# Performance work log

Measured on AMD Instinct MI355X. Metric: run time of the kernel, lower is better.

## Reference

```python
import jax, jax.numpy as jnp
import numpy as np

N_EMBD = 384
NUM_HEADS = 6
HEAD_SIZE = 64


def setup_inputs() -> dict:
    key = jax.random.key(0)
    ks = jax.random.split(key, 6)
    B, T = 128, 256
    D = NUM_HEADS * HEAD_SIZE  # 384
    x = jax.random.normal(ks[0], (B, T, N_EMBD), dtype=jnp.float32)
    Wk = jax.random.normal(ks[1], (N_EMBD, D), dtype=jnp.float32) * (N_EMBD ** -0.5)
    Wq = jax.random.normal(ks[2], (N_EMBD, D), dtype=jnp.float32) * (N_EMBD ** -0.5)
    Wv = jax.random.normal(ks[3], (N_EMBD, D), dtype=jnp.float32) * (N_EMBD ** -0.5)
    Wp = jax.random.normal(ks[4], (D, N_EMBD), dtype=jnp.float32) * (D ** -0.5)
    bp = jax.random.normal(ks[5], (N_EMBD,), dtype=jnp.float32) * 0.01
    return {"x": x, "Wk": Wk, "Wq": Wq, "Wv": Wv, "Wp": Wp, "bp": bp}


def reference(x, Wk, Wq, Wv, Wp, bp):
    B, T, C = x.shape
    H, hs = NUM_HEADS, HEAD_SIZE
    # QKV projections -> [B, H, T, hs]
    q = (x @ Wq).reshape(B, T, H, hs).transpose(0, 2, 1, 3)
    k = (x @ Wk).reshape(B, T, H, hs).transpose(0, 2, 1, 3)
    v = (x @ Wv).reshape(B, T, H, hs).transpose(0, 2, 1, 3)
    # NOTE: original scales by C**-0.5 where C = n_embd (not head_size)
    scale = jnp.asarray(C, x.dtype) ** -0.5
    wei = jnp.einsum('bhtd,bhsd->bhts', q, k) * scale  # [B, H, T, T]
    causal = jnp.tril(jnp.ones((T, T), dtype=bool))
    wei = jnp.where(causal, wei, -jnp.inf)
    wei = jax.nn.softmax(wei, axis=-1)
    # dropout disabled (eval mode) for deterministic reference
    out = jnp.einsum('bhts,bhsd->bhtd', wei, v)  # [B, H, T, hs]
    out = out.transpose(0, 2, 1, 3).reshape(B, T, H * hs)
    return out @ Wp + bp
```

## Files before the change

kernel.cpp:

```cpp
#include <hip/hip_runtime.h>
#include <hip/hip_bf16.h>


#define T_SEQ 256
#define NH 6
#define HS 64
#define CIN 384
#define BATCH 128
#define BT (BATCH * T_SEQ)
#define ELEMS ((size_t)BT * CIN)

using f32x4  = __attribute__((ext_vector_type(4))) float;
using bf16x8 = __attribute__((ext_vector_type(8))) short;

typedef __attribute__((address_space(3))) void       lds_vp;
typedef __attribute__((address_space(1))) const void glob_vp;

static __device__ __forceinline__ unsigned short f2bf(float f) {
  union { float f; unsigned u; } v; v.f = f;
  unsigned r = v.u + 0x7FFFu + ((v.u >> 16) & 1u);
  return (unsigned short)(r >> 16);
}

static __device__ __forceinline__ bf16x8 ld_bf8(const unsigned short* p) {
  return *reinterpret_cast<const bf16x8*>(p);
}

static __device__ __forceinline__ void gl_lds16(const void* g, void* l) {
  __builtin_amdgcn_global_load_lds((glob_vp*)g, (lds_vp*)l, 16, 0, 0);
}

__global__ __launch_bounds__(256) void convert_x(
    const float* __restrict__ x, unsigned short* __restrict__ xb)
{
  size_t i = (((size_t)blockIdx.x << 8) + threadIdx.x) << 3;
  float4 f0 = *reinterpret_cast<const float4*>(x + i);
  float4 f1 = *reinterpret_cast<const float4*>(x + i + 4);
  uint4 pk;
  pk.x = f2bf(f0.x) | ((unsigned)f2bf(f0.y) << 16);
  pk.y = f2bf(f0.z) | ((unsigned)f2bf(f0.w) << 16);
  pk.z = f2bf(f1.x) | ((unsigned)f2bf(f1.y) << 16);
  pk.w = f2bf(f1.z) | ((unsigned)f2bf(f1.w) << 16);
  *reinterpret_cast<uint4*>(xb + i) = pk;
}

__global__ __launch_bounds__(256) void convert_wqkv(
    const float* __restrict__ Wq, const float* __restrict__ Wk,
    const float* __restrict__ Wv, unsigned short* __restrict__ dst)
{
  __shared__ float t[32][33];
  const int z = blockIdx.z;
  const float* __restrict__ W = (z == 0) ? Wq : (z == 1) ? Wk : Wv;
  const int tx = threadIdx.x & 31, ty = threadIdx.x >> 5;
  const int k0 = blockIdx.x * 32, n0 = blockIdx.y * 32;
#pragma unroll
  for (int i = 0; i < 4; ++i)
    t[ty + 8 * i][tx] = W[(size_t)(k0 + ty + 8 * i) * CIN + n0 + tx];
  __syncthreads();
#pragma unroll
  for (int i = 0; i < 4; ++i)
    dst[((size_t)z * CIN + n0 + ty + 8 * i) * CIN + k0 + tx] =
        f2bf(t[tx][ty + 8 * i]);
}

__global__ __launch_bounds__(256) void transpose_w(
    const float* __restrict__ W, unsigned short* __restrict__ dst)
{
  __shared__ float t[32][33];
  const int tx = threadIdx.x & 31, ty = threadIdx.x >> 5;
  const int k0 = blockIdx.x * 32, n0 = blockIdx.y * 32;
#pragma unroll
  for (int i = 0; i < 4; ++i)
    t[ty + 8 * i][tx] = W[(size_t)(k0 + ty + 8 * i) * CIN + n0 + tx];
  __syncthreads();
#pragma unroll
  for (int i = 0; i < 4; ++i)
    dst[((size_t)(n0 + ty + 8 * i)) * CIN + k0 + tx] = f2bf(t[tx][ty + 8 * i]);
}

__global__ __launch_bounds__(256) void gemm_qkv(
    const unsigned short* __restrict__ xb,
    const unsigned short* __restrict__ wt,
    unsigned short* __restrict__ q_ws, unsigned short* __restrict__ k_ws,
    unsigned short* __restrict__ vT_ws)
{
  __shared__ __align__(16) unsigned short XA[2][128][64];
  __shared__ __align__(16) unsigned short XB[2][128][64];

  const int tid = threadIdx.x;
  const int w = tid >> 6, l = tid & 63, g = l >> 4, c = l & 15;
  const int wr = w >> 1, wc = w & 1;

  const int wid = ((int)blockIdx.x & 7) * 288 + ((int)blockIdx.x >> 3);
  const int n_t = wid % 9, m_t = wid / 9;
  const int m0 = m_t * 128, n0 = n_t * 128;

  f32x4 acc[4][4];
#pragma unroll
  for (int mi = 0; mi < 4; ++mi)
#pragma unroll
    for (int nj = 0; nj < 4; ++nj) { f32x4 zz = {0.f,0.f,0.f,0.f}; acc[mi][nj] = zz; }

  const int lrow = l >> 3;
  const int lchk = (l & 7) ^ lrow;
  const char* ga = (const char*)xb +
      ((size_t)(m0 + w * 32 + lrow) * CIN + lchk * 8) * 2;
  const char* gb = (const char*)wt +
      ((size_t)(n0 + w * 32 + lrow) * CIN + lchk * 8) * 2;

#define STAGE_QKV(buf, k0)                                              \
  {                                                                     \
    _Pragma("unroll")                                                   \
    for (int i_ = 0; i_ < 4; ++i_) {                                    \
      gl_lds16(ga + ((k0) + i_ * 8 * CIN) * 2, &XA[buf][w * 32 + i_ * 8][0]); \
      gl_lds16(gb + ((k0) + i_ * 8 * CIN) * 2, &XB[buf][w * 32 + i_ * 8][0]); \
    }                                                                   \
  }

  STAGE_QKV(0, 0);
  __syncthreads();

  int cur = 0;
  for (int t = 0; t < 6; ++t) {
    if (t < 5) STAGE_QKV(cur ^ 1, (t + 1) * 64);
#pragma unroll
    for (int kk = 0; kk < 2; ++kk) {
      bf16x8 a[4], b[4];
#pragma unroll
      for (int mi = 0; mi < 4; ++mi) {
        const int row = wr * 64 + mi * 16 + c;
        a[mi] = *reinterpret_cast<const bf16x8*>(
            (const char*)&XA[cur][row][0] + (((kk * 4 + g) ^ (c & 7)) << 4));
      }
#pragma unroll
      for (int nj = 0; nj < 4; ++nj) {
        const int row = wc * 64 + nj * 16 + c;
        b[nj] = *reinterpret_cast<const bf16x8*>(
            (const char*)&XB[cur][row][0] + (((kk * 4 + g) ^ (c & 7)) << 4));
      }
#pragma unroll
      for (int mi = 0; mi < 4; ++mi)
#pragma unroll
        for (int nj = 0; nj < 4; ++nj)
          acc[mi][nj] = __builtin_amdgcn_mfma_f32_16x16x32_bf16(
              a[mi], b[nj], acc[mi][nj], 0, 0, 0);
    }
    __syncthreads();
    cur ^= 1;
  }

  const int z = n_t / 3;
  const int colw = (n_t % 3) * 128 + wc * 64;
  const int h = colw >> 6;
  const int b = m0 >> 8;
  const int trow0 = (m0 & 255) + wr * 64;

  if (z == 2) {
#pragma unroll
    for (int nj = 0; nj < 4; ++nj) {
      const int d = nj * 16 + c;
#pragma unroll
      for (int mi = 0; mi < 4; ++mi) {
        const int t0 = trow0 + mi * 16 + 4 * g;
        ushort4 pk;
        pk.x = f2bf(acc[mi][nj][0]); pk.y = f2bf(acc[mi][nj][1]);
        pk.z = f2bf(acc[mi][nj][2]); pk.w = f2bf(acc[mi][nj][3]);
        *reinterpret_cast<ushort4*>(
            vT_ws + (((size_t)b * NH + h) * HS + d) * T_SEQ + t0) = pk;
      }
    }
  } else {
    unsigned short* dstb = (z == 0) ? q_ws : k_ws;
    char* OS = (char*)XA + w * 8192;
#pragma unroll
    for (int nj = 0; nj < 4; ++nj)
#pragma unroll
      for (int mi = 0; mi < 4; ++mi)
#pragma unroll
        for (int i = 0; i < 4; ++i) {
          const int r = mi * 16 + 4 * g + i;
          const int chk = (nj * 2 + (c >> 3)) ^ (r & 7);
          *reinterpret_cast<unsigned short*>(
              OS + r * 128 + (chk << 4) + (c & 7) * 2) = f2bf(acc[mi][nj][i]);
        }
    __syncthreads();
    unsigned short* gdst = dstb + (((size_t)b * NH + h) * T_SEQ + trow0) * HS;
#pragma unroll
    for (int p = 0; p < 8; ++p) {
      const int r = p * 8 + (l >> 3);
      const int chk = (l & 7) ^ (r & 7);
      uint4 v = *reinterpret_cast<const uint4*>(OS + r * 128 + (chk << 4));
      *reinterpret_cast<uint4*>((char*)gdst + r * 128 + (l & 7) * 16) = v;
    }
  }
#undef STAGE_QKV
}

template<int NT>
__device__ __forceinline__ void attn_tile(
    const unsigned short* __restrict__ qg,
    const unsigned short* KL, const unsigned short* VL,
    unsigned short* __restrict__ o_ws, int bh, int qt, int g, int c)
{
  const int q0 = qt * 16;
  const int kxor = (c & 7) << 4;

  const char* qrow = (const char*)qg + (size_t)(q0 + c) * 128;
  const bf16x8 qb0 = *reinterpret_cast<const bf16x8*>(qrow + g * 16);
  const bf16x8 qb1 = *reinterpret_cast<const bf16x8*>(qrow + 64 + g * 16);

  f32x4 s[NT];
#pragma unroll
  for (int kt = 0; kt < NT; ++kt) {
    const char* krow = (const char*)KL + (kt * 16 + c) * 128;
    bf16x8 ka0 = *reinterpret_cast<const bf16x8*>(krow + ((g * 16) ^ kxor));
    bf16x8 ka1 = *reinterpret_cast<const bf16x8*>(krow + ((64 + g * 16) ^ kxor));
    f32x4 z = {0.f, 0.f, 0.f, 0.f};
    z = __builtin_amdgcn_mfma_f32_16x16x32_bf16(ka0, qb0, z, 0, 0, 0);
    z = __builtin_amdgcn_mfma_f32_16x16x32_bf16(ka1, qb1, z, 0, 0, 0);
    s[kt] = z;
  }

  const float sc = 0.07362372251839260f;
  float mx = -1e30f;
#pragma unroll
  for (int kt = 0; kt < NT; ++kt)
#pragma unroll
    for (int i = 0; i < 4; ++i) {
      const int k = kt * 16 + 4 * g + i;
      float v = (k <= q0 + c) ? s[kt][i] * sc : -1e30f;
      s[kt][i] = v;
      mx = fmaxf(mx, v);
    }
  mx = fmaxf(mx, __shfl_xor(mx, 16));
  mx = fmaxf(mx, __shfl_xor(mx, 32));

  float sum = 0.f;
#pragma unroll
  for (int kt = 0; kt < NT; ++kt)
#pragma unroll
    for (int i = 0; i < 4; ++i) {
      float p = __builtin_exp2f(s[kt][i] - mx);
      s[kt][i] = p;
      sum += p;
    }
  sum += __shfl_xor(sum, 16);
  sum += __shfl_xor(sum, 32);
  const float inv = 1.0f / sum;

  unsigned pk0[NT], pk1[NT];
#pragma unroll
  for (int kt = 0; kt < NT; ++kt) {
    float2 p01 = {s[kt][0] * inv, s[kt][1] * inv};
    float2 p23 = {s[kt][2] * inv, s[kt][3] * inv};
    __hip_bfloat162 b01 = __float22bfloat162_rn(p01);
    __hip_bfloat162 b23 = __float22bfloat162_rn(p23);
    pk0[kt] = *reinterpret_cast<unsigned*>(&b01);
    pk1[kt] = *reinterpret_cast<unsigned*>(&b23);
  }

  f32x4 acc[4];
#pragma unroll
  for (int nt = 0; nt < 4; ++nt) { f32x4 zz = {0.f,0.f,0.f,0.f}; acc[nt] = zz; }

  const int srcA = ((g & 1) << 5) + c;
  const int srcB = srcA + 16;
  const bool hi = (g >= 2);
#pragma unroll
  for (int ks = 0; ks < NT / 2; ++ks) {
    unsigned a0A = __shfl(pk0[2 * ks],     srcA);
    unsigned a1A = __shfl(pk1[2 * ks],     srcA);
    unsigned a0B = __shfl(pk0[2 * ks],     srcB);
    unsigned a1B = __shfl(pk1[2 * ks],     srcB);
    unsigned b0A = __shfl(pk0[2 * ks + 1], srcA);
    unsigned b1A = __shfl(pk1[2 * ks + 1], srcA);
    unsigned b0B = __shfl(pk0[2 * ks + 1], srcB);
    unsigned b1B = __shfl(pk1[2 * ks + 1], srcB);
    union { unsigned u[4]; bf16x8 v; } pa;
    pa.u[0] = hi ? b0A : a0A;
    pa.u[1] = hi ? b1A : a1A;
    pa.u[2] = hi ? b0B : a0B;
    pa.u[3] = hi ? b1B : a1B;
#pragma unroll
    for (int nt = 0; nt < 4; ++nt) {
      const char* vrow = (const char*)VL + (nt * 16 + c) * 512;
      bf16x8 vb = *reinterpret_cast<const bf16x8*>(
          vrow + ((ks * 64 + g * 16) ^ kxor));
      acc[nt] = __builtin_amdgcn_mfma_f32_16x16x32_bf16(pa.v, vb, acc[nt], 0, 0, 0);
    }
  }

  const int b = bh / NH, h = bh % NH;
  unsigned short* ob = o_ws + ((size_t)(b * T_SEQ + q0)) * CIN + h * HS;
#pragma unroll
  for (int nt = 0; nt < 4; ++nt)
#pragma unroll
    for (int i = 0; i < 4; ++i)
      ob[(size_t)(4 * g + i) * CIN + nt * 16 + c] = f2bf(acc[nt][i]);
}

__global__ __launch_bounds__(512, 4) void attn_kernel(
    const unsigned short* __restrict__ q_ws,
    const unsigned short* __restrict__ k_ws,
    const unsigned short* __restrict__ vT_ws,
    unsigned short* __restrict__ o_ws)
{
  __shared__ __align__(16) unsigned short KL[256 * 64];
  __shared__ __align__(16) unsigned short VL[64 * 256];

  const int tid = threadIdx.x;
  const int w = tid >> 6, l = tid & 63, g = l >> 4, c = l & 15;
  const int bh = blockIdx.x;

  const char* kg = (const char*)(k_ws + (size_t)bh * T_SEQ * HS);
  const char* vg = (const char*)(vT_ws + (size_t)bh * HS * T_SEQ);
#pragma unroll
  for (int i = 0; i < 4; ++i) {
    const int cid = i * 512 + w * 64 + l;
    const int rk = cid >> 3, pk_ = cid & 7;
    gl_lds16(kg + rk * 128 + ((pk_ ^ (rk & 7)) << 4),
             (char*)KL + (size_t)(i * 512 + w * 64) * 16);
    const int rv = cid >> 5, pv = cid & 31;
    const int sv = (pv & ~7) | ((pv & 7) ^ (rv & 7));
    gl_lds16(vg + rv * 512 + (sv << 4),
             (char*)VL + (size_t)(i * 512 + w * 64) * 16);
  }
  __syncthreads();

  const unsigned short* qg = q_ws + (size_t)bh * T_SEQ * HS;
  switch (w) {
    case 0: attn_tile<2>(qg, KL, VL, o_ws, bh, 0, g, c);
            attn_tile<16>(qg, KL, VL, o_ws, bh, 15, g, c); break;
    case 1: attn_tile<2>(qg, KL, VL, o_ws, bh, 1, g, c);
            attn_tile<16>(qg, KL, VL, o_ws, bh, 14, g, c); break;
    case 2: attn_tile<4>(qg, KL, VL, o_ws, bh, 2, g, c);
            attn_tile<14>(qg, KL, VL, o_ws, bh, 13, g, c); break;
    case 3: attn_tile<4>(qg, KL, VL, o_ws, bh, 3, g, c);
            attn_tile<14>(qg, KL, VL, o_ws, bh, 12, g, c); break;
    case 4: attn_tile<6>(qg, KL, VL, o_ws, bh, 4, g, c);
            attn_tile<12>(qg, KL, VL, o_ws, bh, 11, g, c); break;
    case 5: attn_tile<6>(qg, KL, VL, o_ws, bh, 5, g, c);
            attn_tile<12>(qg, KL, VL, o_ws, bh, 10, g, c); break;
    case 6: attn_tile<8>(qg, KL, VL, o_ws, bh, 6, g, c);
            attn_tile<10>(qg, KL, VL, o_ws, bh, 9, g, c); break;
    case 7: attn_tile<8>(qg, KL, VL, o_ws, bh, 7, g, c);
            attn_tile<10>(qg, KL, VL, o_ws, bh, 8, g, c); break;
  }
}

__global__ __launch_bounds__(256) void proj_kernel(
    const unsigned short* __restrict__ ob,
    const unsigned short* __restrict__ wpt,
    const float* __restrict__ bp,
    float* __restrict__ out)
{
  __shared__ __align__(16) unsigned short XA[2][128][64];
  __shared__ __align__(16) unsigned short XB[2][128][64];

  const int tid = threadIdx.x;
  const int w = tid >> 6, l = tid & 63, g = l >> 4, c = l & 15;
  const int wr = w >> 1, wc = w & 1;

  const int wid = ((int)blockIdx.x & 7) * 96 + ((int)blockIdx.x >> 3);
  const int n_t = wid % 3, m_t = wid / 3;
  const int m0 = m_t * 128, n0 = n_t * 128;

  f32x4 acc[4][4];
#pragma unroll
  for (int mi = 0; mi < 4; ++mi)
#pragma unroll
    for (int nj = 0; nj < 4; ++nj) { f32x4 zz = {0.f,0.f,0.f,0.f}; acc[mi][nj] = zz; }

  const int lrow = l >> 3;
  const int lchk = (l & 7) ^ lrow;
  const char* ga = (const char*)ob +
      ((size_t)(m0 + w * 32 + lrow) * CIN + lchk * 8) * 2;
  const char* gb = (const char*)wpt +
      ((size_t)(n0 + w * 32 + lrow) * CIN + lchk * 8) * 2;

#define STAGE_PRJ(buf, k0)                                              \
  {                                                                     \
    _Pragma("unroll")                                                   \
    for (int i_ = 0; i_ < 4; ++i_) {                                    \
      gl_lds16(ga + ((k0) + i_ * 8 * CIN) * 2, &XA[buf][w * 32 + i_ * 8][0]); \
      gl_lds16(gb + ((k0) + i_ * 8 * CIN) * 2, &XB[buf][w * 32 + i_ * 8][0]); \
    }                                                                   \
  }

  STAGE_PRJ(0, 0);
  __syncthreads();

  int cur = 0;
  for (int t = 0; t < 6; ++t) {
    if (t < 5) STAGE_PRJ(cur ^ 1, (t + 1) * 64);
#pragma unroll
    for (int kk = 0; kk < 2; ++kk) {
      bf16x8 a[4], b[4];
#pragma unroll
      for (int mi = 0; mi < 4; ++mi) {
        const int row = wr * 64 + mi * 16 + c;
        a[mi] = *reinterpret_cast<const bf16x8*>(
            (const char*)&XA[cur][row][0] + (((kk * 4 + g) ^ (c & 7)) << 4));
      }
#pragma unroll
      for (int nj = 0; nj < 4; ++nj) {
        const int row = wc * 64 + nj * 16 + c;
        b[nj] = *reinterpret_cast<const bf16x8*>(
            (const char*)&XB[cur][row][0] + (((kk * 4 + g) ^ (c & 7)) << 4));
      }
#pragma unroll
      for (int mi = 0; mi < 4; ++mi)
#pragma unroll
        for (int nj = 0; nj < 4; ++nj)
          acc[mi][nj] = __builtin_amdgcn_mfma_f32_16x16x32_bf16(
              a[mi], b[nj], acc[mi][nj], 0, 0, 0);
    }
    __syncthreads();
    cur ^= 1;
  }

#pragma unroll
  for (int nj = 0; nj < 4; ++nj) {
    const int col = n0 + wc * 64 + nj * 16 + c;
    const float bias = bp[col];
#pragma unroll
    for (int mi = 0; mi < 4; ++mi) {
      const int mrow = m0 + wr * 64 + mi * 16 + 4 * g;
#pragma unroll
      for (int i = 0; i < 4; ++i)
        out[(size_t)(mrow + i) * CIN + col] = acc[mi][nj][i] + bias;
    }
  }
#undef STAGE_PRJ
}

extern "C" void kernel_launch(void* const* d_in, const int* in_sizes, int n_in,
                              void* d_out, int out_size, void* d_ws, size_t ws_size,
                              hipStream_t stream)
{
  const float* x  = (const float*)d_in[0];
  const float* Wk = (const float*)d_in[1];
  const float* Wq = (const float*)d_in[2];
  const float* Wv = (const float*)d_in[3];
  const float* Wp = (const float*)d_in[4];
  const float* bp = (const float*)d_in[5];
  float* out = (float*)d_out;

  unsigned short* ws    = (unsigned short*)d_ws;
  unsigned short* xb_o  = ws;
  unsigned short* q_ws  = ws + ELEMS;
  unsigned short* k_ws  = ws + 2 * ELEMS;
  unsigned short* vT_ws = ws + 3 * ELEMS;
  unsigned short* wqkvT = (unsigned short*)d_out;

  convert_x   <<<6144, 256, 0, stream>>>(x, xb_o);
  convert_wqkv<<<dim3(12, 12, 3), 256, 0, stream>>>(Wq, Wk, Wv, wqkvT);
  gemm_qkv    <<<2304, 256, 0, stream>>>(xb_o, wqkvT, q_ws, k_ws, vT_ws);
  attn_kernel <<<BATCH * NH, 512, 0, stream>>>(q_ws, k_ws, vT_ws, xb_o);
  transpose_w <<<dim3(12, 12), 256, 0, stream>>>(Wp, q_ws);
  proj_kernel <<<768, 256, 0, stream>>>(xb_o, q_ws, bp, out);
}
```

Measured before the change: 119.9 us.

## Single-buffer GEMM LDS tiles and raise wave priority around MFMA blocks

Both GEMM kernels drop double-buffered LDS staging in favour of a single 32KB buffer: each k-step loads, syncs, computes and syncs again. This halves LDS use per block so more blocks can be resident per CU, relying on inter-block overlap to hide load latency instead of intra-block prefetch. s_setprio(1) is also wrapped around the MFMA sequences in the GEMMs and the attention tile to favour issuing matrix ops. The risk is exposed global-to-LDS latency within each block when occupancy does not rise enough to cover it.

```diff
diff --git a/kernel.cpp b/kernel.cpp
--- a/kernel.cpp
+++ b/kernel.cpp
@@ -84,8 +84,7 @@
     unsigned short* __restrict__ q_ws, unsigned short* __restrict__ k_ws,
     unsigned short* __restrict__ vT_ws)
 {
-  __shared__ __align__(16) unsigned short XA[2][128][64];
-  __shared__ __align__(16) unsigned short XB[2][128][64];
+  __shared__ __align__(16) unsigned short SM[2][128][64];
 
   const int tid = threadIdx.x;
   const int w = tid >> 6, l = tid & 63, g = l >> 4, c = l & 15;
@@ -108,21 +107,13 @@
   const char* gb = (const char*)wt +
       ((size_t)(n0 + w * 32 + lrow) * CIN + lchk * 8) * 2;
 
-#define STAGE_QKV(buf, k0)                                              \
-  {                                                                     \
-    _Pragma("unroll")                                                   \
-    for (int i_ = 0; i_ < 4; ++i_) {                                    \
-      gl_lds16(ga + ((k0) + i_ * 8 * CIN) * 2, &XA[buf][w * 32 + i_ * 8][0]); \
-      gl_lds16(gb + ((k0) + i_ * 8 * CIN) * 2, &XB[buf][w * 32 + i_ * 8][0]); \
-    }                                                                   \
-  }
-
-  STAGE_QKV(0, 0);
-  __syncthreads();
-
-  int cur = 0;
   for (int t = 0; t < 6; ++t) {
-    if (t < 5) STAGE_QKV(cur ^ 1, (t + 1) * 64);
+#pragma unroll
+    for (int i_ = 0; i_ < 4; ++i_) {
+      gl_lds16(ga + (t * 64 + i_ * 8 * CIN) * 2, &SM[0][w * 32 + i_ * 8][0]);
+      gl_lds16(gb + (t * 64 + i_ * 8 * CIN) * 2, &SM[1][w * 32 + i_ * 8][0]);
+    }
+    __syncthreads();
 #pragma unroll
     for (int kk = 0; kk < 2; ++kk) {
       bf16x8 a[4], b[4];
@@ -130,23 +121,24 @@
       for (int mi = 0; mi < 4; ++mi) {
         const int row = wr * 64 + mi * 16 + c;
         a[mi] = *reinterpret_cast<const bf16x8*>(
-            (const char*)&XA[cur][row][0] + (((kk * 4 + g) ^ (c & 7)) << 4));
+            (const char*)&SM[0][row][0] + (((kk * 4 + g) ^ (c & 7)) << 4));
       }
 #pragma unroll
       for (int nj = 0; nj < 4; ++nj) {
         const int row = wc * 64 + nj * 16 + c;
         b[nj] = *reinterpret_cast<const bf16x8*>(
-            (const char*)&XB[cur][row][0] + (((kk * 4 + g) ^ (c & 7)) << 4));
+            (const char*)&SM[1][row][0] + (((kk * 4 + g) ^ (c & 7)) << 4));
       }
+      __builtin_amdgcn_s_setprio(1);
 #pragma unroll
       for (int mi = 0; mi < 4; ++mi)
 #pragma unroll
         for (int nj = 0; nj < 4; ++nj)
           acc[mi][nj] = __builtin_amdgcn_mfma_f32_16x16x32_bf16(
               a[mi], b[nj], acc[mi][nj], 0, 0, 0);
+      __builtin_amdgcn_s_setprio(0);
     }
     __syncthreads();
-    cur ^= 1;
   }
 
   const int z = n_t / 3;
@@ -171,7 +163,7 @@
     }
   } else {
     unsigned short* dstb = (z == 0) ? q_ws : k_ws;
-    char* OS = (char*)XA + w * 8192;
+    char* OS = (char*)SM + w * 8192;
 #pragma unroll
     for (int nj = 0; nj < 4; ++nj)
 #pragma unroll
@@ -193,7 +185,6 @@
       *reinterpret_cast<uint4*>((char*)gdst + r * 128 + (l & 7) * 16) = v;
     }
   }
-#undef STAGE_QKV
 }
 
 template<int NT>
@@ -216,8 +207,10 @@
     bf16x8 ka0 = *reinterpret_cast<const bf16x8*>(krow + ((g * 16) ^ kxor));
     bf16x8 ka1 = *reinterpret_cast<const bf16x8*>(krow + ((64 + g * 16) ^ kxor));
     f32x4 z = {0.f, 0.f, 0.f, 0.f};
+    __builtin_amdgcn_s_setprio(1);
     z = __builtin_amdgcn_mfma_f32_16x16x32_bf16(ka0, qb0, z, 0, 0, 0);
     z = __builtin_amdgcn_mfma_f32_16x16x32_bf16(ka1, qb1, z, 0, 0, 0);
+    __builtin_amdgcn_s_setprio(0);
     s[kt] = z;
   }
 
@@ -281,6 +274,7 @@
     pa.u[1] = hi ? b1A : a1A;
     pa.u[2] = hi ? b0B : a0B;
     pa.u[3] = hi ? b1B : a1B;
+    __builtin_amdgcn_s_setprio(1);
 #pragma unroll
     for (int nt = 0; nt < 4; ++nt) {
       const char* vrow = (const char*)VL + (nt * 16 + c) * 512;
@@ -288,6 +282,7 @@
           vrow + ((ks * 64 + g * 16) ^ kxor));
       acc[nt] = __builtin_amdgcn_mfma_f32_16x16x32_bf16(pa.v, vb, acc[nt], 0, 0, 0);
     }
+    __builtin_amdgcn_s_setprio(0);
   }
 
   const int b = bh / NH, h = bh % NH;
@@ -354,8 +349,7 @@
     const float* __restrict__ bp,
     float* __restrict__ out)
 {
-  __shared__ __align__(16) unsigned short XA[2][128][64];
-  __shared__ __align__(16) unsigned short XB[2][128][64];
+  __shared__ __align__(16) unsigned short SM[2][128][64];
 
   const int tid = threadIdx.x;
   const int w = tid >> 6, l = tid & 63, g = l >> 4, c = l & 15;
@@ -378,21 +372,13 @@
   const char* gb = (const char*)wpt +
       ((size_t)(n0 + w * 32 + lrow) * CIN + lchk * 8) * 2;
 
-#define STAGE_PRJ(buf, k0)                                              \
-  {                                                                     \
-    _Pragma("unroll")                                                   \
-    for (int i_ = 0; i_ < 4; ++i_) {                                    \
-      gl_lds16(ga + ((k0) + i_ * 8 * CIN) * 2, &XA[buf][w * 32 + i_ * 8][0]); \
-      gl_lds16(gb + ((k0) + i_ * 8 * CIN) * 2, &XB[buf][w * 32 + i_ * 8][0]); \
-    }                                                                   \
-  }
-
-  STAGE_PRJ(0, 0);
-  __syncthreads();
-
-  int cur = 0;
   for (int t = 0; t < 6; ++t) {
-    if (t < 5) STAGE_PRJ(cur ^ 1, (t + 1) * 64);
+#pragma unroll
+    for (int i_ = 0; i_ < 4; ++i_) {
+      gl_lds16(ga + (t * 64 + i_ * 8 * CIN) * 2, &SM[0][w * 32 + i_ * 8][0]);
+      gl_lds16(gb + (t * 64 + i_ * 8 * CIN) * 2, &SM[1][w * 32 + i_ * 8][0]);
+    }
+    __syncthreads();
 #pragma unroll
     for (int kk = 0; kk < 2; ++kk) {
       bf16x8 a[4], b[4];
@@ -400,23 +386,24 @@
       for (int mi = 0; mi < 4; ++mi) {
         const int row = wr * 64 + mi * 16 + c;
         a[mi] = *reinterpret_cast<const bf16x8*>(
-            (const char*)&XA[cur][row][0] + (((kk * 4 + g) ^ (c & 7)) << 4));
+            (const char*)&SM[0][row][0] + (((kk * 4 + g) ^ (c & 7)) << 4));
       }
 #pragma unroll
       for (int nj = 0; nj < 4; ++nj) {
         const int row = wc * 64 + nj * 16 + c;
         b[nj] = *reinterpret_cast<const bf16x8*>(
-            (const char*)&XB[cur][row][0] + (((kk * 4 + g) ^ (c & 7)) << 4));
+            (const char*)&SM[1][row][0] + (((kk * 4 + g) ^ (c & 7)) << 4));
       }
+      __builtin_amdgcn_s_setprio(1);
 #pragma unroll
       for (int mi = 0; mi < 4; ++mi)
 #pragma unroll
         for (int nj = 0; nj < 4; ++nj)
           acc[mi][nj] = __builtin_amdgcn_mfma_f32_16x16x32_bf16(
               a[mi], b[nj], acc[mi][nj], 0, 0, 0);
+      __builtin_amdgcn_s_setprio(0);
     }
     __syncthreads();
-    cur ^= 1;
   }
 
 #pragma unroll
@@ -431,7 +418,6 @@
         out[(size_t)(mrow + i) * CIN + col] = acc[mi][nj][i] + bias;
     }
   }
-#undef STAGE_PRJ
 }
 
 extern "C" void kernel_launch(void* const* d_in, const int* in_sizes, int n_in,
```

New measurement: 115.8 us. 3.4% less time.

## Fuse fp32-to-bf16 conversion of x into QKV GEMM A-tile loads; add MFMA priority hints

Applied to the files above, without the earlier changes.

Drops the standalone convert_x kernel. The QKV GEMM now loads fp32 x into registers, packs it to bf16 and writes it into swizzled LDS after the MFMAs, while B still uses direct global-to-LDS loads. This removes one kernel launch and a full bf16 write and read of x. In exchange, each of the nine N-tiles rereads fp32 x (twice the bytes) and register pressure rises. It also wraps the MFMA sections in s_setprio in the GEMMs and the attention kernel.

```diff
diff --git a/kernel.cpp b/kernel.cpp
--- a/kernel.cpp
+++ b/kernel.cpp
@@ -22,26 +22,17 @@
   return (unsigned short)(r >> 16);
 }
 
-static __device__ __forceinline__ bf16x8 ld_bf8(const unsigned short* p) {
-  return *reinterpret_cast<const bf16x8*>(p);
-}
-
-static __device__ __forceinline__ void gl_lds16(const void* g, void* l) {
-  __builtin_amdgcn_global_load_lds((glob_vp*)g, (lds_vp*)l, 16, 0, 0);
-}
-
-__global__ __launch_bounds__(256) void convert_x(
-    const float* __restrict__ x, unsigned short* __restrict__ xb)
-{
-  size_t i = (((size_t)blockIdx.x << 8) + threadIdx.x) << 3;
-  float4 f0 = *reinterpret_cast<const float4*>(x + i);
-  float4 f1 = *reinterpret_cast<const float4*>(x + i + 4);
+static __device__ __forceinline__ uint4 pack8(float4 f0, float4 f1) {
   uint4 pk;
   pk.x = f2bf(f0.x) | ((unsigned)f2bf(f0.y) << 16);
   pk.y = f2bf(f0.z) | ((unsigned)f2bf(f0.w) << 16);
   pk.z = f2bf(f1.x) | ((unsigned)f2bf(f1.y) << 16);
   pk.w = f2bf(f1.z) | ((unsigned)f2bf(f1.w) << 16);
-  *reinterpret_cast<uint4*>(xb + i) = pk;
+  return pk;
+}
+
+static __device__ __forceinline__ void gl_lds16(const void* g, void* l) {
+  __builtin_amdgcn_global_load_lds((glob_vp*)g, (lds_vp*)l, 16, 0, 0);
 }
 
 __global__ __launch_bounds__(256) void convert_wqkv(
@@ -79,13 +70,13 @@
 }
 
 __global__ __launch_bounds__(256) void gemm_qkv(
-    const unsigned short* __restrict__ xb,
+    const float* __restrict__ x,
     const unsigned short* __restrict__ wt,
     unsigned short* __restrict__ q_ws, unsigned short* __restrict__ k_ws,
     unsigned short* __restrict__ vT_ws)
 {
-  __shared__ __align__(16) unsigned short XA[2][128][64];
-  __shared__ __align__(16) unsigned short XB[2][128][64];
+  __shared__ __align__(16) unsigned short A [2][128][64];
+  __shared__ __align__(16) unsigned short Bt[2][128][64];
 
   const int tid = threadIdx.x;
   const int w = tid >> 6, l = tid & 63, g = l >> 4, c = l & 15;
@@ -101,28 +92,45 @@
 #pragma unroll
     for (int nj = 0; nj < 4; ++nj) { f32x4 zz = {0.f,0.f,0.f,0.f}; acc[mi][nj] = zz; }
 
-  const int lrow = l >> 3;
-  const int lchk = (l & 7) ^ lrow;
-  const char* ga = (const char*)xb +
-      ((size_t)(m0 + w * 32 + lrow) * CIN + lchk * 8) * 2;
+  const int lr = l >> 3;
+  const int cc = l & 7;
+  const float* gax = x + (size_t)(m0 + w * 32 + lr) * CIN + cc * 8;
   const char* gb = (const char*)wt +
-      ((size_t)(n0 + w * 32 + lrow) * CIN + lchk * 8) * 2;
-
-#define STAGE_QKV(buf, k0)                                              \
-  {                                                                     \
-    _Pragma("unroll")                                                   \
-    for (int i_ = 0; i_ < 4; ++i_) {                                    \
-      gl_lds16(ga + ((k0) + i_ * 8 * CIN) * 2, &XA[buf][w * 32 + i_ * 8][0]); \
-      gl_lds16(gb + ((k0) + i_ * 8 * CIN) * 2, &XB[buf][w * 32 + i_ * 8][0]); \
-    }                                                                   \
-  }
-
-  STAGE_QKV(0, 0);
+      ((size_t)(n0 + w * 32 + lr) * CIN + ((cc ^ lr) << 3)) * 2;
+
+#define ISSUE_B(buf, t)                                                  \
+  _Pragma("unroll")                                                      \
+  for (int i_ = 0; i_ < 4; ++i_)                                         \
+    gl_lds16(gb + ((t) * 64 + i_ * 8 * CIN) * 2, &Bt[buf][w * 32 + i_ * 8][0]);
+
+#define LOAD_A(reg, t)                                                   \
+  _Pragma("unroll")                                                      \
+  for (int i_ = 0; i_ < 4; ++i_) {                                       \
+    reg[i_][0] = *reinterpret_cast<const float4*>(gax + (t) * 64 + i_ * 8 * CIN);     \
+    reg[i_][1] = *reinterpret_cast<const float4*>(gax + (t) * 64 + i_ * 8 * CIN + 4); \
+  }
+
+#define WRITE_A(buf, reg)                                                \
+  _Pragma("unroll")                                                      \
+  for (int i_ = 0; i_ < 4; ++i_)                                         \
+    *reinterpret_cast<uint4*>(&A[buf][w * 32 + lr + i_ * 8][(cc ^ lr) << 3]) = \
+        pack8(reg[i_][0], reg[i_][1]);
+
+  {
+    float4 pa[4][2];
+    LOAD_A(pa, 0);
+    ISSUE_B(0, 0);
+    WRITE_A(0, pa);
+  }
   __syncthreads();
 
   int cur = 0;
   for (int t = 0; t < 6; ++t) {
-    if (t < 5) STAGE_QKV(cur ^ 1, (t + 1) * 64);
+    float4 na[4][2];
+    if (t < 5) {
+      LOAD_A(na, t + 1);
+      ISSUE_B(cur ^ 1, t + 1);
+    }
 #pragma unroll
     for (int kk = 0; kk < 2; ++kk) {
       bf16x8 a[4], b[4];
@@ -130,21 +138,24 @@
       for (int mi = 0; mi < 4; ++mi) {
         const int row = wr * 64 + mi * 16 + c;
         a[mi] = *reinterpret_cast<const bf16x8*>(
-            (const char*)&XA[cur][row][0] + (((kk * 4 + g) ^ (c & 7)) << 4));
+            (const char*)&A[cur][row][0] + (((kk * 4 + g) ^ (c & 7)) << 4));
       }
 #pragma unroll
       for (int nj = 0; nj < 4; ++nj) {
         const int row = wc * 64 + nj * 16 + c;
         b[nj] = *reinterpret_cast<const bf16x8*>(
-            (const char*)&XB[cur][row][0] + (((kk * 4 + g) ^ (c & 7)) << 4));
+            (const char*)&Bt[cur][row][0] + (((kk * 4 + g) ^ (c & 7)) << 4));
       }
+      __builtin_amdgcn_s_setprio(1);
 #pragma unroll
       for (int mi = 0; mi < 4; ++mi)
 #pragma unroll
         for (int nj = 0; nj < 4; ++nj)
           acc[mi][nj] = __builtin_amdgcn_mfma_f32_16x16x32_bf16(
               a[mi], b[nj], acc[mi][nj], 0, 0, 0);
-    }
+      __builtin_amdgcn_s_setprio(0);
+    }
+    if (t < 5) { WRITE_A(cur ^ 1, na); }
     __syncthreads();
     cur ^= 1;
   }
@@ -171,7 +182,7 @@
     }
   } else {
     unsigned short* dstb = (z == 0) ? q_ws : k_ws;
-    char* OS = (char*)XA + w * 8192;
+    char* OS = (char*)A + w * 8192;
 #pragma unroll
     for (int nj = 0; nj < 4; ++nj)
 #pragma unroll
@@ -193,7 +204,9 @@
       *reinterpret_cast<uint4*>((char*)gdst + r * 128 + (l & 7) * 16) = v;
     }
   }
-#undef STAGE_QKV
+#undef ISSUE_B
+#undef LOAD_A
+#undef WRITE_A
 }
 
 template<int NT>
@@ -216,8 +229,10 @@
     bf16x8 ka0 = *reinterpret_cast<const bf16x8*>(krow + ((g * 16) ^ kxor));
     bf16x8 ka1 = *reinterpret_cast<const bf16x8*>(krow + ((64 + g * 16) ^ kxor));
     f32x4 z = {0.f, 0.f, 0.f, 0.f};
+    __builtin_amdgcn_s_setprio(1);
     z = __builtin_amdgcn_mfma_f32_16x16x32_bf16(ka0, qb0, z, 0, 0, 0);
     z = __builtin_amdgcn_mfma_f32_16x16x32_bf16(ka1, qb1, z, 0, 0, 0);
+    __builtin_amdgcn_s_setprio(0);
     s[kt] = z;
   }
 
@@ -281,6 +296,7 @@
     pa.u[1] = hi ? b1A : a1A;
     pa.u[2] = hi ? b0B : a0B;
     pa.u[3] = hi ? b1B : a1B;
+    __builtin_amdgcn_s_setprio(1);
 #pragma unroll
     for (int nt = 0; nt < 4; ++nt) {
       const char* vrow = (const char*)VL + (nt * 16 + c) * 512;
@@ -288,6 +304,7 @@
           vrow + ((ks * 64 + g * 16) ^ kxor));
       acc[nt] = __builtin_amdgcn_mfma_f32_16x16x32_bf16(pa.v, vb, acc[nt], 0, 0, 0);
     }
+    __builtin_amdgcn_s_setprio(0);
   }
 
   const int b = bh / NH, h = bh % NH;
@@ -371,19 +388,19 @@
 #pragma unroll
     for (int nj = 0; nj < 4; ++nj) { f32x4 zz = {0.f,0.f,0.f,0.f}; acc[mi][nj] = zz; }
 
-  const int lrow = l >> 3;
-  const int lchk = (l & 7) ^ lrow;
+  const int lr = l >> 3;
+  const int lchk = (l & 7) ^ lr;
   const char* ga = (const char*)ob +
-      ((size_t)(m0 + w * 32 + lrow) * CIN + lchk * 8) * 2;
+      ((size_t)(m0 + w * 32 + lr) * CIN + lchk * 8) * 2;
   const char* gb = (const char*)wpt +
-      ((size_t)(n0 + w * 32 + lrow) * CIN + lchk * 8) * 2;
-
-#define STAGE_PRJ(buf, k0)                                              \
+      ((size_t)(n0 + w * 32 + lr) * CIN + lchk * 8) * 2;
+
+#define STAGE_PRJ(buf, t)                                               \
   {                                                                     \
     _Pragma("unroll")                                                   \
     for (int i_ = 0; i_ < 4; ++i_) {                                    \
-      gl_lds16(ga + ((k0) + i_ * 8 * CIN) * 2, &XA[buf][w * 32 + i_ * 8][0]); \
-      gl_lds16(gb + ((k0) + i_ * 8 * CIN) * 2, &XB[buf][w * 32 + i_ * 8][0]); \
+      gl_lds16(ga + ((t) * 64 + i_ * 8 * CIN) * 2, &XA[buf][w * 32 + i_ * 8][0]); \
+      gl_lds16(gb + ((t) * 64 + i_ * 8 * CIN) * 2, &XB[buf][w * 32 + i_ * 8][0]); \
     }                                                                   \
   }
 
@@ -392,7 +409,7 @@
 
   int cur = 0;
   for (int t = 0; t < 6; ++t) {
-    if (t < 5) STAGE_PRJ(cur ^ 1, (t + 1) * 64);
+    if (t < 5) STAGE_PRJ(cur ^ 1, t + 1);
 #pragma unroll
     for (int kk = 0; kk < 2; ++kk) {
       bf16x8 a[4], b[4];
@@ -408,12 +425,14 @@
         b[nj] = *reinterpret_cast<const bf16x8*>(
             (const char*)&XB[cur][row][0] + (((kk * 4 + g) ^ (c & 7)) << 4));
       }
+      __builtin_amdgcn_s_setprio(1);
 #pragma unroll
       for (int mi = 0; mi < 4; ++mi)
 #pragma unroll
         for (int nj = 0; nj < 4; ++nj)
           acc[mi][nj] = __builtin_amdgcn_mfma_f32_16x16x32_bf16(
               a[mi], b[nj], acc[mi][nj], 0, 0, 0);
+      __builtin_amdgcn_s_setprio(0);
     }
     __syncthreads();
     cur ^= 1;
@@ -447,16 +466,15 @@
   float* out = (float*)d_out;
 
   unsigned short* ws    = (unsigned short*)d_ws;
-  unsigned short* xb_o  = ws;
+  unsigned short* o_ws  = ws;
   unsigned short* q_ws  = ws + ELEMS;
   unsigned short* k_ws  = ws + 2 * ELEMS;
   unsigned short* vT_ws = ws + 3 * ELEMS;
   unsigned short* wqkvT = (unsigned short*)d_out;
 
-  convert_x   <<<6144, 256, 0, stream>>>(x, xb_o);
   convert_wqkv<<<dim3(12, 12, 3), 256, 0, stream>>>(Wq, Wk, Wv, wqkvT);
-  gemm_qkv    <<<2304, 256, 0, stream>>>(xb_o, wqkvT, q_ws, k_ws, vT_ws);
-  attn_kernel <<<BATCH * NH, 512, 0, stream>>>(q_ws, k_ws, vT_ws, xb_o);
+  gemm_qkv    <<<2304, 256, 0, stream>>>(x, wqkvT, q_ws, k_ws, vT_ws);
+  attn_kernel <<<BATCH * NH, 512, 0, stream>>>(q_ws, k_ws, vT_ws, o_ws);
   transpose_w <<<dim3(12, 12), 256, 0, stream>>>(Wp, q_ws);
-  proj_kernel <<<768, 256, 0, stream>>>(xb_o, q_ws, bp, out);
-}
+  proj_kernel <<<768, 256, 0, stream>>>(o_ws, q_ws, bp, out);
+}
```

New measurement: 124.4 us. 1.04x slower.

## Prefetch two K-stages ahead in projection GEMMs and raise MFMA wave priority

Applied to the files above, without the earlier changes.

The QKV and output-projection GEMM main loops are restructured so two K-tiles of global-to-LDS loads are in flight at once. Completion is now gated by explicit `s_waitcnt vmcnt(8)` counts plus raw `s_barrier`, replacing full `__syncthreads` after every step. This is meant to hide more global-load latency behind MFMA work. `s_setprio(1)`/`(0)` brackets around MFMA bursts in the GEMMs and the attention kernel let waves issuing matrix ops get scheduling priority over waves issuing loads. The cost is reliance on hand-counted vmcnt values and scheduling barriers, which break silently if the load count per stage changes.

```diff
diff --git a/kernel.cpp b/kernel.cpp
--- a/kernel.cpp
+++ b/kernel.cpp
@@ -101,53 +101,67 @@
 #pragma unroll
     for (int nj = 0; nj < 4; ++nj) { f32x4 zz = {0.f,0.f,0.f,0.f}; acc[mi][nj] = zz; }
 
-  const int lrow = l >> 3;
-  const int lchk = (l & 7) ^ lrow;
+  const int lr = l >> 3;
+  const int lchk = (l & 7) ^ lr;
   const char* ga = (const char*)xb +
-      ((size_t)(m0 + w * 32 + lrow) * CIN + lchk * 8) * 2;
+      ((size_t)(m0 + w * 32 + lr) * CIN + lchk * 8) * 2;
   const char* gb = (const char*)wt +
-      ((size_t)(n0 + w * 32 + lrow) * CIN + lchk * 8) * 2;
-
-#define STAGE_QKV(buf, k0)                                              \
+      ((size_t)(n0 + w * 32 + lr) * CIN + lchk * 8) * 2;
+
+#define STG(buf, t)                                                     \
   {                                                                     \
     _Pragma("unroll")                                                   \
     for (int i_ = 0; i_ < 4; ++i_) {                                    \
-      gl_lds16(ga + ((k0) + i_ * 8 * CIN) * 2, &XA[buf][w * 32 + i_ * 8][0]); \
-      gl_lds16(gb + ((k0) + i_ * 8 * CIN) * 2, &XB[buf][w * 32 + i_ * 8][0]); \
+      gl_lds16(ga + ((t) * 64 + i_ * 8 * CIN) * 2, &XA[buf][w * 32 + i_ * 8][0]); \
+      gl_lds16(gb + ((t) * 64 + i_ * 8 * CIN) * 2, &XB[buf][w * 32 + i_ * 8][0]); \
     }                                                                   \
   }
 
-  STAGE_QKV(0, 0);
+#define CMP(buf)                                                        \
+  {                                                                     \
+    _Pragma("unroll")                                                   \
+    for (int kk = 0; kk < 2; ++kk) {                                    \
+      bf16x8 a[4], b[4];                                                \
+      _Pragma("unroll")                                                 \
+      for (int mi = 0; mi < 4; ++mi) {                                  \
+        const int row = wr * 64 + mi * 16 + c;                          \
+        a[mi] = *reinterpret_cast<const bf16x8*>(                       \
+            (const char*)&XA[buf][row][0] + (((kk * 4 + g) ^ (c & 7)) << 4)); \
+      }                                                                 \
+      _Pragma("unroll")                                                 \
+      for (int nj = 0; nj < 4; ++nj) {                                  \
+        const int row = wc * 64 + nj * 16 + c;                          \
+        b[nj] = *reinterpret_cast<const bf16x8*>(                       \
+            (const char*)&XB[buf][row][0] + (((kk * 4 + g) ^ (c & 7)) << 4)); \
+      }                                                                 \
+      __builtin_amdgcn_s_setprio(1);                                    \
+      _Pragma("unroll")                                                 \
+      for (int mi = 0; mi < 4; ++mi)                                    \
+        _Pragma("unroll")                                               \
+        for (int nj = 0; nj < 4; ++nj)                                  \
+          acc[mi][nj] = __builtin_amdgcn_mfma_f32_16x16x32_bf16(        \
+              a[mi], b[nj], acc[mi][nj], 0, 0, 0);                      \
+      __builtin_amdgcn_s_setprio(0);                                    \
+    }                                                                   \
+  }
+
+  STG(0, 0);
+  STG(1, 1);
+#pragma unroll 1
+  for (int t = 0; t < 5; ++t) {
+    asm volatile("s_waitcnt vmcnt(8)" ::: "memory");
+    __builtin_amdgcn_s_barrier();
+    __builtin_amdgcn_sched_barrier(0);
+    const int cur = t & 1;
+    CMP(cur);
+    __builtin_amdgcn_s_barrier();
+    if (t < 4) STG(cur, t + 2);
+  }
+  asm volatile("s_waitcnt vmcnt(0)" ::: "memory");
+  __builtin_amdgcn_s_barrier();
+  __builtin_amdgcn_sched_barrier(0);
+  CMP(1);
   __syncthreads();
-
-  int cur = 0;
-  for (int t = 0; t < 6; ++t) {
-    if (t < 5) STAGE_QKV(cur ^ 1, (t + 1) * 64);
-#pragma unroll
-    for (int kk = 0; kk < 2; ++kk) {
-      bf16x8 a[4], b[4];
-#pragma unroll
-      for (int mi = 0; mi < 4; ++mi) {
-        const int row = wr * 64 + mi * 16 + c;
-        a[mi] = *reinterpret_cast<const bf16x8*>(
-            (const char*)&XA[cur][row][0] + (((kk * 4 + g) ^ (c & 7)) << 4));
-      }
-#pragma unroll
-      for (int nj = 0; nj < 4; ++nj) {
-        const int row = wc * 64 + nj * 16 + c;
-        b[nj] = *reinterpret_cast<const bf16x8*>(
-            (const char*)&XB[cur][row][0] + (((kk * 4 + g) ^ (c & 7)) << 4));
-      }
-#pragma unroll
-      for (int mi = 0; mi < 4; ++mi)
-#pragma unroll
-        for (int nj = 0; nj < 4; ++nj)
-          acc[mi][nj] = __builtin_amdgcn_mfma_f32_16x16x32_bf16(
-              a[mi], b[nj], acc[mi][nj], 0, 0, 0);
-    }
-    __syncthreads();
-    cur ^= 1;
-  }
 
   const int z = n_t / 3;
   const int colw = (n_t % 3) * 128 + wc * 64;
@@ -193,7 +207,8 @@
       *reinterpret_cast<uint4*>((char*)gdst + r * 128 + (l & 7) * 16) = v;
     }
   }
-#undef STAGE_QKV
+#undef STG
+#undef CMP
 }
 
 template<int NT>
@@ -216,8 +231,10 @@
     bf16x8 ka0 = *reinterpret_cast<const bf16x8*>(krow + ((g * 16) ^ kxor));
     bf16x8 ka1 = *reinterpret_cast<const bf16x8*>(krow + ((64 + g * 16) ^ kxor));
     f32x4 z = {0.f, 0.f, 0.f, 0.f};
+    __builtin_amdgcn_s_setprio(1);
     z = __builtin_amdgcn_mfma_f32_16x16x32_bf16(ka0, qb0, z, 0, 0, 0);
     z = __builtin_amdgcn_mfma_f32_16x16x32_bf16(ka1, qb1, z, 0, 0, 0);
+    __builtin_amdgcn_s_setprio(0);
     s[kt] = z;
   }
 
@@ -281,6 +298,7 @@
     pa.u[1] = hi ? b1A : a1A;
     pa.u[2] = hi ? b0B : a0B;
     pa.u[3] = hi ? b1B : a1B;
+    __builtin_amdgcn_s_setprio(1);
 #pragma unroll
     for (int nt = 0; nt < 4; ++nt) {
       const char* vrow = (const char*)VL + (nt * 16 + c) * 512;
@@ -288,6 +306,7 @@
           vrow + ((ks * 64 + g * 16) ^ kxor));
       acc[nt] = __builtin_amdgcn_mfma_f32_16x16x32_bf16(pa.v, vb, acc[nt], 0, 0, 0);
     }
+    __builtin_amdgcn_s_setprio(0);
   }
 
   const int b = bh / NH, h = bh % NH;
@@ -371,53 +390,66 @@
 #pragma unroll
     for (int nj = 0; nj < 4; ++nj) { f32x4 zz = {0.f,0.f,0.f,0.f}; acc[mi][nj] = zz; }
 
-  const int lrow = l >> 3;
-  const int lchk = (l & 7) ^ lrow;
+  const int lr = l >> 3;
+  const int lchk = (l & 7) ^ lr;
   const char* ga = (const char*)ob +
-      ((size_t)(m0 + w * 32 + lrow) * CIN + lchk * 8) * 2;
+      ((size_t)(m0 + w * 32 + lr) * CIN + lchk * 8) * 2;
   const char* gb = (const char*)wpt +
-      ((size_t)(n0 + w * 32 + lrow) * CIN + lchk * 8) * 2;
-
-#define STAGE_PRJ(buf, k0)                                              \
+      ((size_t)(n0 + w * 32 + lr) * CIN + lchk * 8) * 2;
+
+#define STG(buf, t)                                                     \
   {                                                                     \
     _Pragma("unroll")                                                   \
     for (int i_ = 0; i_ < 4; ++i_) {                                    \
-      gl_lds16(ga + ((k0) + i_ * 8 * CIN) * 2, &XA[buf][w * 32 + i_ * 8][0]); \
-      gl_lds16(gb + ((k0) + i_ * 8 * CIN) * 2, &XB[buf][w * 32 + i_ * 8][0]); \
+      gl_lds16(ga + ((t) * 64 + i_ * 8 * CIN) * 2, &XA[buf][w * 32 + i_ * 8][0]); \
+      gl_lds16(gb + ((t) * 64 + i_ * 8 * CIN) * 2, &XB[buf][w * 32 + i_ * 8][0]); \
     }                                                                   \
   }
 
-  STAGE_PRJ(0, 0);
-  __syncthreads();
-
-  int cur = 0;
-  for (int t = 0; t < 6; ++t) {
-    if (t < 5) STAGE_PRJ(cur ^ 1, (t + 1) * 64);
-#pragma unroll
-    for (int kk = 0; kk < 2; ++kk) {
-      bf16x8 a[4], b[4];
-#pragma unroll
-      for (int mi = 0; mi < 4; ++mi) {
-        const int row = wr * 64 + mi * 16 + c;
-        a[mi] = *reinterpret_cast<const bf16x8*>(
-            (const char*)&XA[cur][row][0] + (((kk * 4 + g) ^ (c & 7)) << 4));
-      }
-#pragma unroll
-      for (int nj = 0; nj < 4; ++nj) {
-        const int row = wc * 64 + nj * 16 + c;
-        b[nj] = *reinterpret_cast<const bf16x8*>(
-            (const char*)&XB[cur][row][0] + (((kk * 4 + g) ^ (c & 7)) << 4));
-      }
-#pragma unroll
-      for (int mi = 0; mi < 4; ++mi)
-#pragma unroll
-        for (int nj = 0; nj < 4; ++nj)
-          acc[mi][nj] = __builtin_amdgcn_mfma_f32_16x16x32_bf16(
-              a[mi], b[nj], acc[mi][nj], 0, 0, 0);
-    }
-    __syncthreads();
-    cur ^= 1;
-  }
+#define CMP(buf)                                                        \
+  {                                                                     \
+    _Pragma("unroll")                                                   \
+    for (int kk = 0; kk < 2; ++kk) {                                    \
+      bf16x8 a[4], b[4];                                                \
+      _Pragma("unroll")                                                 \
+      for (int mi = 0; mi < 4; ++mi) {                                  \
+        const int row = wr * 64 + mi * 16 + c;                          \
+        a[mi] = *reinterpret_cast<const bf16x8*>(                       \
+            (const char*)&XA[buf][row][0] + (((kk * 4 + g) ^ (c & 7)) << 4)); \
+      }                                                                 \
+      _Pragma("unroll")                                                 \
+      for (int nj = 0; nj < 4; ++nj) {                                  \
+        const int row = wc * 64 + nj * 16 + c;                          \
+        b[nj] = *reinterpret_cast<const bf16x8*>(                       \
+            (const char*)&XB[buf][row][0] + (((kk * 4 + g) ^ (c & 7)) << 4)); \
+      }                                                                 \
+      __builtin_amdgcn_s_setprio(1);                                    \
+      _Pragma("unroll")                                                 \
+      for (int mi = 0; mi < 4; ++mi)                                    \
+        _Pragma("unroll")                                               \
+        for (int nj = 0; nj < 4; ++nj)                                  \
+          acc[mi][nj] = __builtin_amdgcn_mfma_f32_16x16x32_bf16(        \
+              a[mi], b[nj], acc[mi][nj], 0, 0, 0);                      \
+      __builtin_amdgcn_s_setprio(0);                                    \
+    }                                                                   \
+  }
+
+  STG(0, 0);
+  STG(1, 1);
+#pragma unroll 1
+  for (int t = 0; t < 5; ++t) {
+    asm volatile("s_waitcnt vmcnt(8)" ::: "memory");
+    __builtin_amdgcn_s_barrier();
+    __builtin_amdgcn_sched_barrier(0);
+    const int cur = t & 1;
+    CMP(cur);
+    __builtin_amdgcn_s_barrier();
+    if (t < 4) STG(cur, t + 2);
+  }
+  asm volatile("s_waitcnt vmcnt(0)" ::: "memory");
+  __builtin_amdgcn_s_barrier();
+  __builtin_amdgcn_sched_barrier(0);
+  CMP(1);
 
 #pragma unroll
   for (int nj = 0; nj < 4; ++nj) {
@@ -431,7 +463,8 @@
         out[(size_t)(mrow + i) * CIN + col] = acc[mi][nj][i] + bias;
     }
   }
-#undef STAGE_PRJ
+#undef STG
+#undef CMP
 }
 
 extern "C" void kernel_launch(void* const* d_in, const int* in_sizes, int n_in,
```

New measurement: 110.6 us. 7.7% less time.
